# Performance work log

Measured on AMD Instinct MI355X. Metric: run time of the kernel, lower is better.

The kernel has to match this reference:

```python
import jax, jax.numpy as jnp
import numpy as np

N = 100000
E = 1600000
F_NODE = 6
F_EDGE = 2
H = 64


def _glorot(key, shape):
    lim = float(np.sqrt(6.0 / (shape[0] + shape[1])))
    return jax.random.uniform(key, shape, jnp.float32, -lim, lim)


def setup_inputs() -> dict:
    key = jax.random.key(0)
    ks = jax.random.split(key, 16)
    inp = {
        "x": jax.random.normal(ks[0], (N, F_NODE), jnp.float32),
        "edge_index": jax.random.randint(ks[1], (2, E), 0, N, jnp.int64),
        "edge_attr": jax.random.normal(ks[2], (E, F_EDGE), jnp.float32),
        # GCN layers (PyG GCNConv: linear no-bias, then aggregate, then +bias)
        "W1": _glorot(ks[3], (F_NODE, H)), "b1": jnp.zeros((H,), jnp.float32),
        "W2": _glorot(ks[4], (H, H)), "b2": jnp.zeros((H,), jnp.float32),
        "W3": _glorot(ks[5], (H, H)), "b3": jnp.zeros((H,), jnp.float32),
        # edge_mlp
        "We1": _glorot(ks[6], (F_EDGE, H)), "be1": jnp.zeros((H,), jnp.float32),
        "We2": _glorot(ks[7], (H, H)), "be2": jnp.zeros((H,), jnp.float32),
        # predictor
        "Wp1": _glorot(ks[8], (3 * H, H)), "bp1": jnp.zeros((H,), jnp.float32),
        "Wp2": _glorot(ks[9], (H, H // 2)), "bp2": jnp.zeros((H // 2,), jnp.float32),
        "Wp3": _glorot(ks[10], (H // 2, 1)), "bp3": jnp.zeros((1,), jnp.float32),
    }
    return inp


def _gcn_conv(h, W, b, src_sl, dst_sl, norm, n):
    # PyG GCNConv with self-loops and symmetric normalization
    h = h @ W                                   # [N, H_out]
    msg = h[src_sl] * norm[:, None]             # gather + scale per edge(+loop)
    out = jax.ops.segment_sum(msg, dst_sl, num_segments=n)
    return out + b


def _forward(x, edge_attr, W1, b1, W2, b2, W3, b3, We1, be1, We2, be2,
             Wp1, bp1, Wp2, bp2, Wp3, bp3, edge_index):
    n = x.shape[0]
    src, dst = edge_index[0], edge_index[1]

    # --- edge feature injection (vectorized version of per-edge loop) ---
    ef = jax.nn.relu(edge_attr @ We1 + be1) @ We2 + be2      # [E, H]
    nef = (jax.ops.segment_sum(ef, src, num_segments=n)
           + jax.ops.segment_sum(ef, dst, num_segments=n))   # [N, H]
    ones_e = jnp.ones((ef.shape[0],), x.dtype)
    deg = (jax.ops.segment_sum(ones_e, src, num_segments=n)
           + jax.ops.segment_sum(ones_e, dst, num_segments=n))
    deg = jnp.maximum(deg, 1.0)
    nef = nef / deg[:, None]
    # hidden_dim (64) >= node feature dim (6) -> truncate
    x = x + nef[:, : x.shape[1]] * 0.5

    # --- GCN normalization with self-loops (shared across layers) ---
    loop = jnp.arange(n, dtype=src.dtype)
    src_sl = jnp.concatenate([src, loop])
    dst_sl = jnp.concatenate([dst, loop])
    deg_sl = jax.ops.segment_sum(jnp.ones_like(dst_sl, dtype=x.dtype), dst_sl,
                                 num_segments=n)
    dinv = jnp.where(deg_sl > 0, deg_sl ** -0.5, 0.0)
    norm = dinv[src_sl] * dinv[dst_sl]

    h = jax.nn.relu(_gcn_conv(x, W1, b1, src_sl, dst_sl, norm, n))
    h = jax.nn.relu(_gcn_conv(h, W2, b2, src_sl, dst_sl, norm, n))
    h = _gcn_conv(h, W3, b3, src_sl, dst_sl, norm, n)

    graph_emb = h.mean(axis=0)                 # global_mean_pool, batch=None
    node_mean = h.mean(axis=0)
    node_std = jnp.std(h, axis=0, ddof=1)      # torch.std is unbiased
    combined = jnp.concatenate([graph_emb, node_mean, node_std])  # [3H]

    p = jax.nn.relu(combined @ Wp1 + bp1)      # dropout inactive in eval
    p = jax.nn.relu(p @ Wp2 + bp2)
    out = jax.nn.sigmoid(p @ Wp3 + bp3)        # (1,)
    return out


def reference(x, edge_index, edge_attr, W1, b1, W2, b2, W3, b3,
              We1, be1, We2, be2, Wp1, bp1, Wp2, bp2, Wp3, bp3):
    return _forward(x, edge_attr, W1, b1, W2, b2, W3, b3, We1, be1, We2, be2,
                    Wp1, bp1, Wp2, bp2, Wp3, bp3, edge_index)
```

## Files before the change

kernel.cpp:

```cpp
#include <hip/hip_runtime.h>
#include <hip/hip_bf16.h>
#include <stdint.h>

#define CSTRIDE 8

__device__ __forceinline__ float rdlane(float v, int l) {
    return __uint_as_float(__builtin_amdgcn_readlane(__float_as_uint(v), l));
}
__device__ __forceinline__ float bf2f(unsigned short u) {
    return __uint_as_float(((unsigned)u) << 16);
}
__device__ __forceinline__ unsigned short f2bf(float f) {
    unsigned u = __float_as_uint(f);
    u += 0x7fffu + ((u >> 16) & 1u);
    return (unsigned short)(u >> 16);
}
__device__ __forceinline__ unsigned packbf(float a, float b) {
    return (unsigned)f2bf(a) | ((unsigned)f2bf(b) << 16);
}

__global__ void k_zero(int* __restrict__ cntO, int* __restrict__ cntI,
                       double* __restrict__ sums, int n) {
    int i = blockIdx.x * blockDim.x + threadIdx.x;
    if (i < 128) sums[i] = 0.0;
    if (i < n) { cntO[(size_t)i * CSTRIDE] = 0; cntI[(size_t)i * CSTRIDE] = 0; }
}

__global__ __launch_bounds__(256) void k_front(
    const int* __restrict__ ei, const float* __restrict__ ea,
    const float* __restrict__ We1, const float* __restrict__ be1,
    const float* __restrict__ We2, const float* __restrict__ be2,
    unsigned* __restrict__ efp, int* __restrict__ cntO, int* __restrict__ cntI,
    int* __restrict__ rankS, int* __restrict__ rankD, int E) {
    __shared__ float sWe1[128], sbe1[64], sWe2[64 * 6], sbe2[6];
    int t = threadIdx.x;
    if (t < 128) sWe1[t] = We1[t];
    if (t < 64) {
        sbe1[t] = be1[t];
#pragma unroll
        for (int c = 0; c < 6; ++c) sWe2[t * 6 + c] = We2[t * 64 + c];
    }
    if (t < 6) sbe2[t] = be2[t];
    __syncthreads();

    int e = blockIdx.x * blockDim.x + t;
    if (e >= E) return;

    int s = ei[e], d = ei[E + e];
    int rs = atomicAdd(&cntO[(size_t)s * CSTRIDE], 1);
    int rd = atomicAdd(&cntI[(size_t)d * CSTRIDE], 1);

    float2 aa = ((const float2*)ea)[e];
    float a0 = aa.x, a1 = aa.y;
    float acc[6];
#pragma unroll
    for (int c = 0; c < 6; ++c) acc[c] = sbe2[c];
#pragma unroll
    for (int j = 0; j < 64; ++j) {
        float h = fmaf(a0, sWe1[j], fmaf(a1, sWe1[64 + j], sbe1[j]));
        h = fmaxf(h, 0.f);
#pragma unroll
        for (int c = 0; c < 6; ++c) acc[c] = fmaf(h, sWe2[j * 6 + c], acc[c]);
    }
    unsigned* q = efp + (size_t)e * 3;
    q[0] = packbf(acc[0], acc[1]);
    q[1] = packbf(acc[2], acc[3]);
    q[2] = packbf(acc[4], acc[5]);
    rankS[e] = rs;
    rankD[e] = rd;
}

__global__ __launch_bounds__(256) void k_scan1(const int* __restrict__ cntO,
                                               const int* __restrict__ cntI,
                                               int2* __restrict__ bsum, int n) {
    __shared__ int2 l[256];
    int i = blockIdx.x * 256 + threadIdx.x;
    l[threadIdx.x] = (i < n) ? make_int2(cntO[(size_t)i * CSTRIDE],
                                         cntI[(size_t)i * CSTRIDE])
                             : make_int2(0, 0);
    __syncthreads();
    for (int s = 128; s > 0; s >>= 1) {
        if (threadIdx.x < s) {
            l[threadIdx.x].x += l[threadIdx.x + s].x;
            l[threadIdx.x].y += l[threadIdx.x + s].y;
        }
        __syncthreads();
    }
    if (threadIdx.x == 0) bsum[blockIdx.x] = l[0];
}

__global__ __launch_bounds__(512) void k_scan2(int2* __restrict__ bsum, int nb,
                                               int* __restrict__ offON,
                                               int* __restrict__ offIN) {
    __shared__ int2 l[512];
    int t = threadIdx.x;
    int2 v = (t < nb) ? bsum[t] : make_int2(0, 0);
    l[t] = v;
    __syncthreads();
    for (int s = 1; s < 512; s <<= 1) {
        int2 tmp = (t >= s) ? l[t - s] : make_int2(0, 0);
        __syncthreads();
        l[t].x += tmp.x; l[t].y += tmp.y;
        __syncthreads();
    }
    if (t < nb) bsum[t] = make_int2(l[t].x - v.x, l[t].y - v.y);
    if (t == 511) { *offON = l[511].x; *offIN = l[511].y; }
}

__global__ __launch_bounds__(256) void k_scan3off(const int* __restrict__ cntO,
                                                  const int* __restrict__ cntI,
                                                  const int2* __restrict__ bsum,
                                                  int* __restrict__ offO,
                                                  int* __restrict__ offI, int n) {
    __shared__ int2 l[256];
    int i = blockIdx.x * 256 + threadIdx.x;
    int2 v = (i < n) ? make_int2(cntO[(size_t)i * CSTRIDE],
                                 cntI[(size_t)i * CSTRIDE])
                     : make_int2(0, 0);
    l[threadIdx.x] = v;
    __syncthreads();
    for (int s = 1; s < 256; s <<= 1) {
        int2 tmp = (threadIdx.x >= (unsigned)s) ? l[threadIdx.x - s] : make_int2(0, 0);
        __syncthreads();
        l[threadIdx.x].x += tmp.x; l[threadIdx.x].y += tmp.y;
        __syncthreads();
    }
    if (i < n) {
        int2 bs = bsum[blockIdx.x];
        offO[i] = l[threadIdx.x].x - v.x + bs.x;
        offI[i] = l[threadIdx.x].y - v.y + bs.y;
    }
}

__global__ __launch_bounds__(256) void k_place(const int* __restrict__ ei,
                                               const int* __restrict__ rankS,
                                               const int* __restrict__ rankD,
                                               const int* __restrict__ offO,
                                               const int* __restrict__ offI,
                                               unsigned* __restrict__ out_eid,
                                               uint2* __restrict__ in_pk, int E) {
    int e = blockIdx.x * blockDim.x + threadIdx.x;
    if (e >= E) return;
    int s = ei[e], d = ei[E + e];
    out_eid[offO[s] + rankS[e]] = (unsigned)e;
    in_pk[offI[d] + rankD[e]] = make_uint2((unsigned)s, (unsigned)e);
}

__global__ __launch_bounds__(256) void k_nef_x(
    const int* __restrict__ offO, const unsigned* __restrict__ out_eid,
    const int* __restrict__ offI, const uint2* __restrict__ in_pk,
    const unsigned* __restrict__ efp, const float* __restrict__ x,
    float* __restrict__ xp, float* __restrict__ dinv, int n) {
    int i = blockIdx.x * blockDim.x + threadIdx.x;
    if (i >= n) return;
    int bo = offO[i], eo = offO[i + 1];
    int bi = offI[i], eiN = offI[i + 1];
    float a0 = 0.f, a1 = 0.f, a2 = 0.f, a3 = 0.f, a4 = 0.f, a5 = 0.f;
    for (int j = bo; j < eo; ++j) {
        const unsigned* q = efp + (size_t)out_eid[j] * 3;
        unsigned u0 = q[0], u1 = q[1], u2 = q[2];
        a0 += bf2f((unsigned short)u0); a1 += bf2f((unsigned short)(u0 >> 16));
        a2 += bf2f((unsigned short)u1); a3 += bf2f((unsigned short)(u1 >> 16));
        a4 += bf2f((unsigned short)u2); a5 += bf2f((unsigned short)(u2 >> 16));
    }
    for (int j = bi; j < eiN; ++j) {
        const unsigned* q = efp + (size_t)in_pk[j].y * 3;
        unsigned u0 = q[0], u1 = q[1], u2 = q[2];
        a0 += bf2f((unsigned short)u0); a1 += bf2f((unsigned short)(u0 >> 16));
        a2 += bf2f((unsigned short)u1); a3 += bf2f((unsigned short)(u1 >> 16));
        a4 += bf2f((unsigned short)u2); a5 += bf2f((unsigned short)(u2 >> 16));
    }
    int indeg = eiN - bi;
    float degf = (float)((eo - bo) + indeg);
    float inv = 0.5f / fmaxf(degf, 1.f);
    xp[(size_t)i * 6 + 0] = x[(size_t)i * 6 + 0] + a0 * inv;
    xp[(size_t)i * 6 + 1] = x[(size_t)i * 6 + 1] + a1 * inv;
    xp[(size_t)i * 6 + 2] = x[(size_t)i * 6 + 2] + a2 * inv;
    xp[(size_t)i * 6 + 3] = x[(size_t)i * 6 + 3] + a3 * inv;
    xp[(size_t)i * 6 + 4] = x[(size_t)i * 6 + 4] + a4 * inv;
    xp[(size_t)i * 6 + 5] = x[(size_t)i * 6 + 5] + a5 * inv;
    dinv[i] = 1.f / sqrtf(1.f + (float)indeg);
}

__global__ __launch_bounds__(256) void k_mm1(const float* __restrict__ xp,
                                             const float* __restrict__ W1,
                                             const float* __restrict__ dinv,
                                             unsigned short* __restrict__ sOut, int n) {
    int lane = threadIdx.x & 63;
    int wid = (blockIdx.x * blockDim.x + threadIdx.x) >> 6;
    int nw = (gridDim.x * blockDim.x) >> 6;
    float w[6];
#pragma unroll
    for (int c = 0; c < 6; ++c) w[c] = W1[c * 64 + lane];
    for (int i = wid; i < n; i += nw) {
        float xv = (lane < 6) ? xp[(size_t)i * 6 + lane] : 0.f;
        float acc = 0.f;
#pragma unroll
        for (int c = 0; c < 6; ++c) acc = fmaf(rdlane(xv, c), w[c], acc);
        sOut[(size_t)i * 64 + lane] = f2bf(acc * dinv[i]);
    }
}

__global__ __launch_bounds__(256) void k_gathermm(
    const int* __restrict__ offI, const uint2* __restrict__ in_pk,
    const float* __restrict__ dinv, const unsigned short* __restrict__ sIn,
    const float* __restrict__ bias, const float* __restrict__ W,
    unsigned short* __restrict__ sOut, int n) {
    int lane = threadIdx.x & 63;
    int sub = lane & 15, grp = lane >> 4;
    int wid = (blockIdx.x * blockDim.x + threadIdx.x) >> 6;
    int nw = (gridDim.x * blockDim.x) >> 6;
    float w[64];
#pragma unroll
    for (int c = 0; c < 64; ++c) w[c] = W[c * 64 + lane];
    float4 bb = ((const float4*)bias)[sub];

    for (int i = wid; i < n; i += nw) {
        ushort4 sv = *(const ushort4*)(sIn + (size_t)i * 64 + sub * 4);
        float a0, a1, a2, a3;
        if (grp == 0) { a0 = bf2f(sv.x); a1 = bf2f(sv.y); a2 = bf2f(sv.z); a3 = bf2f(sv.w); }
        else { a0 = a1 = a2 = a3 = 0.f; }
        int b0 = offI[i], e0 = offI[i + 1];
#pragma unroll 4
        for (int j = b0 + grp; j < e0; j += 4) {
            unsigned src = in_pk[j].x;
            ushort4 v = *(const ushort4*)(sIn + (size_t)src * 64 + sub * 4);
            a0 += bf2f(v.x); a1 += bf2f(v.y); a2 += bf2f(v.z); a3 += bf2f(v.w);
        }
        a0 += __shfl_xor(a0, 16); a1 += __shfl_xor(a1, 16);
        a2 += __shfl_xor(a2, 16); a3 += __shfl_xor(a3, 16);
        a0 += __shfl_xor(a0, 32); a1 += __shfl_xor(a1, 32);
        a2 += __shfl_xor(a2, 32); a3 += __shfl_xor(a3, 32);

        float dv = dinv[i];
        float h0 = fmaxf(fmaf(a0, dv, bb.x), 0.f);
        float h1 = fmaxf(fmaf(a1, dv, bb.y), 0.f);
        float h2 = fmaxf(fmaf(a2, dv, bb.z), 0.f);
        float h3 = fmaxf(fmaf(a3, dv, bb.w), 0.f);
        float o = 0.f;
#pragma unroll
        for (int g = 0; g < 16; ++g) {
            o = fmaf(rdlane(h0, g), w[g * 4 + 0], o);
            o = fmaf(rdlane(h1, g), w[g * 4 + 1], o);
            o = fmaf(rdlane(h2, g), w[g * 4 + 2], o);
            o = fmaf(rdlane(h3, g), w[g * 4 + 3], o);
        }
        sOut[(size_t)i * 64 + lane] = f2bf(o * dv);
    }
}

__global__ __launch_bounds__(256) void k_gatherreduce(
    const int* __restrict__ offI, const uint2* __restrict__ in_pk,
    const float* __restrict__ dinv, const unsigned short* __restrict__ sIn,
    const float* __restrict__ b3, double* __restrict__ sums, int n) {
    int lane = threadIdx.x & 63;
    int sub = lane & 15, grp = lane >> 4;
    int wv = threadIdx.x >> 6;
    int wid = (blockIdx.x * blockDim.x + threadIdx.x) >> 6;
    int nw = (gridDim.x * blockDim.x) >> 6;
    float4 bb = ((const float4*)b3)[sub];
    double s0 = 0.0, s1 = 0.0, s2_ = 0.0, s3 = 0.0;
    double q0 = 0.0, q1 = 0.0, q2 = 0.0, q3 = 0.0;

    for (int i = wid; i < n; i += nw) {
        ushort4 sv = *(const ushort4*)(sIn + (size_t)i * 64 + sub * 4);
        float a0, a1, a2, a3;
        if (grp == 0) { a0 = bf2f(sv.x); a1 = bf2f(sv.y); a2 = bf2f(sv.z); a3 = bf2f(sv.w); }
        else { a0 = a1 = a2 = a3 = 0.f; }
        int b0 = offI[i], e0 = offI[i + 1];
#pragma unroll 4
        for (int j = b0 + grp; j < e0; j += 4) {
            unsigned src = in_pk[j].x;
            ushort4 v = *(const ushort4*)(sIn + (size_t)src * 64 + sub * 4);
            a0 += bf2f(v.x); a1 += bf2f(v.y); a2 += bf2f(v.z); a3 += bf2f(v.w);
        }
        a0 += __shfl_xor(a0, 16); a1 += __shfl_xor(a1, 16);
        a2 += __shfl_xor(a2, 16); a3 += __shfl_xor(a3, 16);
        a0 += __shfl_xor(a0, 32); a1 += __shfl_xor(a1, 32);
        a2 += __shfl_xor(a2, 32); a3 += __shfl_xor(a3, 32);

        float dv = dinv[i];
        float v0 = fmaf(a0, dv, bb.x);
        float v1 = fmaf(a1, dv, bb.y);
        float v2 = fmaf(a2, dv, bb.z);
        float v3 = fmaf(a3, dv, bb.w);
        s0 += v0; s1 += v1; s2_ += v2; s3 += v3;
        q0 += (double)v0 * v0; q1 += (double)v1 * v1;
        q2 += (double)v2 * v2; q3 += (double)v3 * v3;
    }
    __shared__ double shS[4 * 64], shQ[4 * 64];
    if (grp == 0) {
#pragma unroll
        for (int k = 0; k < 4; ++k) {
            double sk = (k == 0) ? s0 : (k == 1) ? s1 : (k == 2) ? s2_ : s3;
            double qk = (k == 0) ? q0 : (k == 1) ? q1 : (k == 2) ? q2 : q3;
            shS[wv * 64 + sub * 4 + k] = sk;
            shQ[wv * 64 + sub * 4 + k] = qk;
        }
    }
    __syncthreads();
    if (wv == 0) {
        double a = shS[lane] + shS[64 + lane] + shS[128 + lane] + shS[192 + lane];
        double c = shQ[lane] + shQ[64 + lane] + shQ[128 + lane] + shQ[192 + lane];
        unsafeAtomicAdd(&sums[lane], a);
        unsafeAtomicAdd(&sums[64 + lane], c);
    }
}

__global__ void k_head(const double* __restrict__ sums,
                       const float* __restrict__ Wp1, const float* __restrict__ bp1,
                       const float* __restrict__ Wp2, const float* __restrict__ bp2,
                       const float* __restrict__ Wp3, const float* __restrict__ bp3,
                       float* __restrict__ out, int n) {
    __shared__ float comb[192], p1[64], p2[32];
    int t = threadIdx.x;
    if (t < 64) {
        double s = sums[t], s2 = sums[64 + t];
        double m = s / n;
        double var = (s2 - s * s / n) / (double)(n - 1);
        float mf = (float)m;
        float sd = (float)sqrt(var > 0.0 ? var : 0.0);
        comb[t] = mf;
        comb[64 + t] = mf;
        comb[128 + t] = sd;
    }
    __syncthreads();
    if (t < 64) {
        float acc = bp1[t];
        for (int k = 0; k < 192; ++k) acc = fmaf(comb[k], Wp1[k * 64 + t], acc);
        p1[t] = fmaxf(acc, 0.f);
    }
    __syncthreads();
    if (t < 32) {
        float acc = bp2[t];
        for (int k = 0; k < 64; ++k) acc = fmaf(p1[k], Wp2[k * 32 + t], acc);
        p2[t] = fmaxf(acc, 0.f);
    }
    __syncthreads();
    if (t == 0) {
        float acc = bp3[0];
        for (int k = 0; k < 32; ++k) acc = fmaf(p2[k], Wp3[k], acc);
        out[0] = 1.f / (1.f + expf(-acc));
    }
}

static inline char* align16(char* p) {
    return (char*)(((uintptr_t)p + 15) & ~(uintptr_t)15);
}

extern "C" void kernel_launch(void* const* d_in, const int* in_sizes, int n_in,
                              void* d_out, int out_size, void* d_ws, size_t ws_size,
                              hipStream_t stream) {
    const float* x   = (const float*)d_in[0];
    const int*   ei  = (const int*)d_in[1];
    const float* ea  = (const float*)d_in[2];
    const float* W1  = (const float*)d_in[3];
    const float* b1  = (const float*)d_in[4];
    const float* W2  = (const float*)d_in[5];
    const float* b2  = (const float*)d_in[6];
    const float* W3  = (const float*)d_in[7];
    const float* b3  = (const float*)d_in[8];
    const float* We1 = (const float*)d_in[9];
    const float* be1 = (const float*)d_in[10];
    const float* We2 = (const float*)d_in[11];
    const float* be2 = (const float*)d_in[12];
    const float* Wp1 = (const float*)d_in[13];
    const float* bp1 = (const float*)d_in[14];
    const float* Wp2 = (const float*)d_in[15];
    const float* bp2 = (const float*)d_in[16];
    const float* Wp3 = (const float*)d_in[17];
    const float* bp3 = (const float*)d_in[18];

    const int N = in_sizes[0] / 6;
    const int E = in_sizes[1] / 2;
    const int nbN = (N + 255) / 256;
    const int nbE = (E + 255) / 256;
    const size_t SB = (size_t)N * 64 * 2;

    char* p = (char*)d_ws;
    double* sums = (double*)p;          p = align16(p + 128 * sizeof(double));
    int* cntO = (int*)p;                p = align16(p + (size_t)N * CSTRIDE * 4);
    int* cntI = (int*)p;                p = align16(p + (size_t)N * CSTRIDE * 4);
    int* offO = (int*)p;                p = align16(p + ((size_t)N + 1) * 4);
    int* offI = (int*)p;                p = align16(p + ((size_t)N + 1) * 4);
    int2* bsum = (int2*)p;              p = align16(p + 512 * 8);
    float* xp = (float*)p;              p = align16(p + (size_t)N * 6 * 4);
    float* dinv = (float*)p;            p = align16(p + (size_t)N * 4);
    uint2* in_pk = (uint2*)p;           p = align16(p + (size_t)E * 8);
    char* u1 = p;                       p = align16(p + 2 * SB);
    int* rankS = (int*)u1;
    int* rankD = (int*)(u1 + SB);
    unsigned short* sbufA = (unsigned short*)u1;
    unsigned short* sbufB = (unsigned short*)(u1 + SB);
    char* u2 = p;
    unsigned* efp = (unsigned*)u2;
    unsigned* out_eid = (unsigned*)(u2 + (size_t)E * 12);

    const int TB = 256;
    dim3 blk(TB);

    k_zero<<<dim3(nbN), blk, 0, stream>>>(cntO, cntI, sums, N);
    k_front<<<dim3(nbE), blk, 0, stream>>>(ei, ea, We1, be1, We2, be2,
                                           efp, cntO, cntI, rankS, rankD, E);
    k_scan1<<<dim3(nbN), blk, 0, stream>>>(cntO, cntI, bsum, N);
    k_scan2<<<dim3(1), dim3(512), 0, stream>>>(bsum, nbN, offO + N, offI + N);
    k_scan3off<<<dim3(nbN), blk, 0, stream>>>(cntO, cntI, bsum, offO, offI, N);
    k_place<<<dim3(nbE), blk, 0, stream>>>(ei, rankS, rankD, offO, offI, out_eid, in_pk, E);
    k_nef_x<<<dim3(nbN), blk, 0, stream>>>(offO, out_eid, offI, in_pk, efp, x, xp, dinv, N);

    k_mm1<<<dim3(1024), blk, 0, stream>>>(xp, W1, dinv, sbufA, N);
    k_gathermm<<<dim3(2048), blk, 0, stream>>>(offI, in_pk, dinv, sbufA, b1, W2, sbufB, N);
    k_gathermm<<<dim3(2048), blk, 0, stream>>>(offI, in_pk, dinv, sbufB, b2, W3, sbufA, N);
    k_gatherreduce<<<dim3(2048), blk, 0, stream>>>(offI, in_pk, dinv, sbufA, b3, sums, N);
    k_head<<<dim3(1), dim3(64), 0, stream>>>(sums, Wp1, bp1, Wp2, bp2, Wp3, bp3,
                                             (float*)d_out, N);
}
```

Measured before the change: 593.9 us.

## Store GCN node features in fp8, inline edge features into CSR records

Node feature buffers for the GCN gathers switch from bf16 to packed fp8 (4 values per 32-bit word) to halve gather traffic per edge. The placement kernel now copies each edge's packed features into the out- and in-sorted records so the nef pass reads sequentially instead of doing an indirect lookup. The per-node counter padding (stride 8) is removed, so the count arrays become dense. This trades accuracy (fp8 activations) and larger in-records (16 bytes) for less random memory traffic, and dense counters may bring more atomic contention within a cache line.

```diff
diff --git a/kernel.cpp b/kernel.cpp
--- a/kernel.cpp
+++ b/kernel.cpp
@@ -2,7 +2,7 @@
 #include <hip/hip_bf16.h>
 #include <stdint.h>
 
-#define CSTRIDE 8
+typedef float floatx2 __attribute__((ext_vector_type(2)));
 
 __device__ __forceinline__ float rdlane(float v, int l) {
     return __uint_as_float(__builtin_amdgcn_readlane(__float_as_uint(v), l));
@@ -18,12 +18,17 @@
 __device__ __forceinline__ unsigned packbf(float a, float b) {
     return (unsigned)f2bf(a) | ((unsigned)f2bf(b) << 16);
 }
+__device__ __forceinline__ unsigned pk_fp8x4(float a, float b, float c, float d) {
+    int u = __builtin_amdgcn_cvt_pk_fp8_f32(a, b, 0, false);
+    u = __builtin_amdgcn_cvt_pk_fp8_f32(c, d, u, true);
+    return (unsigned)u;
+}
 
 __global__ void k_zero(int* __restrict__ cntO, int* __restrict__ cntI,
                        double* __restrict__ sums, int n) {
     int i = blockIdx.x * blockDim.x + threadIdx.x;
     if (i < 128) sums[i] = 0.0;
-    if (i < n) { cntO[(size_t)i * CSTRIDE] = 0; cntI[(size_t)i * CSTRIDE] = 0; }
+    if (i < n) { cntO[i] = 0; cntI[i] = 0; }
 }
 
 __global__ __launch_bounds__(256) void k_front(
@@ -47,8 +52,8 @@
     if (e >= E) return;
 
     int s = ei[e], d = ei[E + e];
-    int rs = atomicAdd(&cntO[(size_t)s * CSTRIDE], 1);
-    int rd = atomicAdd(&cntI[(size_t)d * CSTRIDE], 1);
+    int rs = atomicAdd(&cntO[s], 1);
+    int rd = atomicAdd(&cntI[d], 1);
 
     float2 aa = ((const float2*)ea)[e];
     float a0 = aa.x, a1 = aa.y;
@@ -75,9 +80,7 @@
                                                int2* __restrict__ bsum, int n) {
     __shared__ int2 l[256];
     int i = blockIdx.x * 256 + threadIdx.x;
-    l[threadIdx.x] = (i < n) ? make_int2(cntO[(size_t)i * CSTRIDE],
-                                         cntI[(size_t)i * CSTRIDE])
-                             : make_int2(0, 0);
+    l[threadIdx.x] = (i < n) ? make_int2(cntO[i], cntI[i]) : make_int2(0, 0);
     __syncthreads();
     for (int s = 128; s > 0; s >>= 1) {
         if (threadIdx.x < s) {
@@ -114,9 +117,7 @@
                                                   int* __restrict__ offI, int n) {
     __shared__ int2 l[256];
     int i = blockIdx.x * 256 + threadIdx.x;
-    int2 v = (i < n) ? make_int2(cntO[(size_t)i * CSTRIDE],
-                                 cntI[(size_t)i * CSTRIDE])
-                     : make_int2(0, 0);
+    int2 v = (i < n) ? make_int2(cntO[i], cntI[i]) : make_int2(0, 0);
     l[threadIdx.x] = v;
     __syncthreads();
     for (int s = 1; s < 256; s <<= 1) {
@@ -137,19 +138,23 @@
                                                const int* __restrict__ rankD,
                                                const int* __restrict__ offO,
                                                const int* __restrict__ offI,
-                                               unsigned* __restrict__ out_eid,
-                                               uint2* __restrict__ in_pk, int E) {
+                                               const unsigned* __restrict__ efp,
+                                               unsigned* __restrict__ out_rec,
+                                               uint4* __restrict__ in_rec, int E) {
     int e = blockIdx.x * blockDim.x + threadIdx.x;
     if (e >= E) return;
     int s = ei[e], d = ei[E + e];
-    out_eid[offO[s] + rankS[e]] = (unsigned)e;
-    in_pk[offI[d] + rankD[e]] = make_uint2((unsigned)s, (unsigned)e);
+    const unsigned* q = efp + (size_t)e * 3;
+    unsigned u0 = q[0], u1 = q[1], u2 = q[2];
+    size_t so = (size_t)(offO[s] + rankS[e]) * 3;
+    out_rec[so] = u0; out_rec[so + 1] = u1; out_rec[so + 2] = u2;
+    in_rec[offI[d] + rankD[e]] = make_uint4((unsigned)s, u0, u1, u2);
 }
 
 __global__ __launch_bounds__(256) void k_nef_x(
-    const int* __restrict__ offO, const unsigned* __restrict__ out_eid,
-    const int* __restrict__ offI, const uint2* __restrict__ in_pk,
-    const unsigned* __restrict__ efp, const float* __restrict__ x,
+    const int* __restrict__ offO, const unsigned* __restrict__ out_rec,
+    const int* __restrict__ offI, const uint4* __restrict__ in_rec,
+    const float* __restrict__ x,
     float* __restrict__ xp, float* __restrict__ dinv, int n) {
     int i = blockIdx.x * blockDim.x + threadIdx.x;
     if (i >= n) return;
@@ -157,18 +162,17 @@
     int bi = offI[i], eiN = offI[i + 1];
     float a0 = 0.f, a1 = 0.f, a2 = 0.f, a3 = 0.f, a4 = 0.f, a5 = 0.f;
     for (int j = bo; j < eo; ++j) {
-        const unsigned* q = efp + (size_t)out_eid[j] * 3;
+        const unsigned* q = out_rec + (size_t)j * 3;
         unsigned u0 = q[0], u1 = q[1], u2 = q[2];
         a0 += bf2f((unsigned short)u0); a1 += bf2f((unsigned short)(u0 >> 16));
         a2 += bf2f((unsigned short)u1); a3 += bf2f((unsigned short)(u1 >> 16));
         a4 += bf2f((unsigned short)u2); a5 += bf2f((unsigned short)(u2 >> 16));
     }
     for (int j = bi; j < eiN; ++j) {
-        const unsigned* q = efp + (size_t)in_pk[j].y * 3;
-        unsigned u0 = q[0], u1 = q[1], u2 = q[2];
-        a0 += bf2f((unsigned short)u0); a1 += bf2f((unsigned short)(u0 >> 16));
-        a2 += bf2f((unsigned short)u1); a3 += bf2f((unsigned short)(u1 >> 16));
-        a4 += bf2f((unsigned short)u2); a5 += bf2f((unsigned short)(u2 >> 16));
+        uint4 r = in_rec[j];
+        a0 += bf2f((unsigned short)r.y); a1 += bf2f((unsigned short)(r.y >> 16));
+        a2 += bf2f((unsigned short)r.z); a3 += bf2f((unsigned short)(r.z >> 16));
+        a4 += bf2f((unsigned short)r.w); a5 += bf2f((unsigned short)(r.w >> 16));
     }
     int indeg = eiN - bi;
     float degf = (float)((eo - bo) + indeg);
@@ -185,8 +189,9 @@
 __global__ __launch_bounds__(256) void k_mm1(const float* __restrict__ xp,
                                              const float* __restrict__ W1,
                                              const float* __restrict__ dinv,
-                                             unsigned short* __restrict__ sOut, int n) {
+                                             unsigned* __restrict__ sOut, int n) {
     int lane = threadIdx.x & 63;
+    int sub = lane & 15;
     int wid = (blockIdx.x * blockDim.x + threadIdx.x) >> 6;
     int nw = (gridDim.x * blockDim.x) >> 6;
     float w[6];
@@ -197,15 +202,20 @@
         float acc = 0.f;
 #pragma unroll
         for (int c = 0; c < 6; ++c) acc = fmaf(rdlane(xv, c), w[c], acc);
-        sOut[(size_t)i * 64 + lane] = f2bf(acc * dinv[i]);
+        float o = acc * dinv[i];
+        float o0 = __shfl(o, sub * 4 + 0);
+        float o1 = __shfl(o, sub * 4 + 1);
+        float o2 = __shfl(o, sub * 4 + 2);
+        float o3 = __shfl(o, sub * 4 + 3);
+        if (lane < 16) sOut[(size_t)i * 16 + lane] = pk_fp8x4(o0, o1, o2, o3);
     }
 }
 
 __global__ __launch_bounds__(256) void k_gathermm(
-    const int* __restrict__ offI, const uint2* __restrict__ in_pk,
-    const float* __restrict__ dinv, const unsigned short* __restrict__ sIn,
+    const int* __restrict__ offI, const uint4* __restrict__ in_rec,
+    const float* __restrict__ dinv, const unsigned* __restrict__ sIn,
     const float* __restrict__ bias, const float* __restrict__ W,
-    unsigned short* __restrict__ sOut, int n) {
+    unsigned* __restrict__ sOut, int n) {
     int lane = threadIdx.x & 63;
     int sub = lane & 15, grp = lane >> 4;
     int wid = (blockIdx.x * blockDim.x + threadIdx.x) >> 6;
@@ -216,16 +226,21 @@
     float4 bb = ((const float4*)bias)[sub];
 
     for (int i = wid; i < n; i += nw) {
-        ushort4 sv = *(const ushort4*)(sIn + (size_t)i * 64 + sub * 4);
+        unsigned su = sIn[(size_t)i * 16 + sub];
         float a0, a1, a2, a3;
-        if (grp == 0) { a0 = bf2f(sv.x); a1 = bf2f(sv.y); a2 = bf2f(sv.z); a3 = bf2f(sv.w); }
-        else { a0 = a1 = a2 = a3 = 0.f; }
+        if (grp == 0) {
+            floatx2 lo = __builtin_amdgcn_cvt_pk_f32_fp8(su, false);
+            floatx2 hi = __builtin_amdgcn_cvt_pk_f32_fp8(su, true);
+            a0 = lo.x; a1 = lo.y; a2 = hi.x; a3 = hi.y;
+        } else { a0 = a1 = a2 = a3 = 0.f; }
         int b0 = offI[i], e0 = offI[i + 1];
 #pragma unroll 4
         for (int j = b0 + grp; j < e0; j += 4) {
-            unsigned src = in_pk[j].x;
-            ushort4 v = *(const ushort4*)(sIn + (size_t)src * 64 + sub * 4);
-            a0 += bf2f(v.x); a1 += bf2f(v.y); a2 += bf2f(v.z); a3 += bf2f(v.w);
+            unsigned src = in_rec[j].x;
+            unsigned u = sIn[(size_t)src * 16 + sub];
+            floatx2 lo = __builtin_amdgcn_cvt_pk_f32_fp8(u, false);
+            floatx2 hi = __builtin_amdgcn_cvt_pk_f32_fp8(u, true);
+            a0 += lo.x; a1 += lo.y; a2 += hi.x; a3 += hi.y;
         }
         a0 += __shfl_xor(a0, 16); a1 += __shfl_xor(a1, 16);
         a2 += __shfl_xor(a2, 16); a3 += __shfl_xor(a3, 16);
@@ -245,13 +260,18 @@
             o = fmaf(rdlane(h2, g), w[g * 4 + 2], o);
             o = fmaf(rdlane(h3, g), w[g * 4 + 3], o);
         }
-        sOut[(size_t)i * 64 + lane] = f2bf(o * dv);
+        o *= dv;
+        float o0 = __shfl(o, sub * 4 + 0);
+        float o1 = __shfl(o, sub * 4 + 1);
+        float o2 = __shfl(o, sub * 4 + 2);
+        float o3 = __shfl(o, sub * 4 + 3);
+        if (lane < 16) sOut[(size_t)i * 16 + lane] = pk_fp8x4(o0, o1, o2, o3);
     }
 }
 
 __global__ __launch_bounds__(256) void k_gatherreduce(
-    const int* __restrict__ offI, const uint2* __restrict__ in_pk,
-    const float* __restrict__ dinv, const unsigned short* __restrict__ sIn,
+    const int* __restrict__ offI, const uint4* __restrict__ in_rec,
+    const float* __restrict__ dinv, const unsigned* __restrict__ sIn,
     const float* __restrict__ b3, double* __restrict__ sums, int n) {
     int lane = threadIdx.x & 63;
     int sub = lane & 15, grp = lane >> 4;
@@ -263,16 +283,21 @@
     double q0 = 0.0, q1 = 0.0, q2 = 0.0, q3 = 0.0;
 
     for (int i = wid; i < n; i += nw) {
-        ushort4 sv = *(const ushort4*)(sIn + (size_t)i * 64 + sub * 4);
+        unsigned su = sIn[(size_t)i * 16 + sub];
         float a0, a1, a2, a3;
-        if (grp == 0) { a0 = bf2f(sv.x); a1 = bf2f(sv.y); a2 = bf2f(sv.z); a3 = bf2f(sv.w); }
-        else { a0 = a1 = a2 = a3 = 0.f; }
+        if (grp == 0) {
+            floatx2 lo = __builtin_amdgcn_cvt_pk_f32_fp8(su, false);
+            floatx2 hi = __builtin_amdgcn_cvt_pk_f32_fp8(su, true);
+            a0 = lo.x; a1 = lo.y; a2 = hi.x; a3 = hi.y;
+        } else { a0 = a1 = a2 = a3 = 0.f; }
         int b0 = offI[i], e0 = offI[i + 1];
 #pragma unroll 4
         for (int j = b0 + grp; j < e0; j += 4) {
-            unsigned src = in_pk[j].x;
-            ushort4 v = *(const ushort4*)(sIn + (size_t)src * 64 + sub * 4);
-            a0 += bf2f(v.x); a1 += bf2f(v.y); a2 += bf2f(v.z); a3 += bf2f(v.w);
+            unsigned src = in_rec[j].x;
+            unsigned u = sIn[(size_t)src * 16 + sub];
+            floatx2 lo = __builtin_amdgcn_cvt_pk_f32_fp8(u, false);
+            floatx2 hi = __builtin_amdgcn_cvt_pk_f32_fp8(u, true);
+            a0 += lo.x; a1 += lo.y; a2 += hi.x; a3 += hi.y;
         }
         a0 += __shfl_xor(a0, 16); a1 += __shfl_xor(a1, 16);
         a2 += __shfl_xor(a2, 16); a3 += __shfl_xor(a3, 16);
@@ -375,26 +400,26 @@
     const int E = in_sizes[1] / 2;
     const int nbN = (N + 255) / 256;
     const int nbE = (E + 255) / 256;
-    const size_t SB = (size_t)N * 64 * 2;
+    const size_t SB = (size_t)N * 64;
 
     char* p = (char*)d_ws;
     double* sums = (double*)p;          p = align16(p + 128 * sizeof(double));
-    int* cntO = (int*)p;                p = align16(p + (size_t)N * CSTRIDE * 4);
-    int* cntI = (int*)p;                p = align16(p + (size_t)N * CSTRIDE * 4);
+    int* cntO = (int*)p;                p = align16(p + (size_t)N * 4);
+    int* cntI = (int*)p;                p = align16(p + (size_t)N * 4);
     int* offO = (int*)p;                p = align16(p + ((size_t)N + 1) * 4);
     int* offI = (int*)p;                p = align16(p + ((size_t)N + 1) * 4);
     int2* bsum = (int2*)p;              p = align16(p + 512 * 8);
     float* xp = (float*)p;              p = align16(p + (size_t)N * 6 * 4);
     float* dinv = (float*)p;            p = align16(p + (size_t)N * 4);
-    uint2* in_pk = (uint2*)p;           p = align16(p + (size_t)E * 8);
-    char* u1 = p;                       p = align16(p + 2 * SB);
+    uint4* in_rec = (uint4*)p;          p = align16(p + (size_t)E * 16);
+    char* u1 = p;                       p = align16(p + 2 * ((SB + 15) & ~(size_t)15));
     int* rankS = (int*)u1;
-    int* rankD = (int*)(u1 + SB);
-    unsigned short* sbufA = (unsigned short*)u1;
-    unsigned short* sbufB = (unsigned short*)(u1 + SB);
+    int* rankD = (int*)(u1 + ((SB + 15) & ~(size_t)15));
+    unsigned* sbufA = (unsigned*)rankS;
+    unsigned* sbufB = (unsigned*)rankD;
     char* u2 = p;
     unsigned* efp = (unsigned*)u2;
-    unsigned* out_eid = (unsigned*)(u2 + (size_t)E * 12);
+    unsigned* out_rec = (unsigned*)(u2 + (size_t)E * 12);
 
     const int TB = 256;
     dim3 blk(TB);
@@ -405,13 +430,14 @@
     k_scan1<<<dim3(nbN), blk, 0, stream>>>(cntO, cntI, bsum, N);
     k_scan2<<<dim3(1), dim3(512), 0, stream>>>(bsum, nbN, offO + N, offI + N);
     k_scan3off<<<dim3(nbN), blk, 0, stream>>>(cntO, cntI, bsum, offO, offI, N);
-    k_place<<<dim3(nbE), blk, 0, stream>>>(ei, rankS, rankD, offO, offI, out_eid, in_pk, E);
-    k_nef_x<<<dim3(nbN), blk, 0, stream>>>(offO, out_eid, offI, in_pk, efp, x, xp, dinv, N);
+    k_place<<<dim3(nbE), blk, 0, stream>>>(ei, rankS, rankD, offO, offI, efp,
+                                           out_rec, in_rec, E);
+    k_nef_x<<<dim3(nbN), blk, 0, stream>>>(offO, out_rec, offI, in_rec, x, xp, dinv, N);
 
     k_mm1<<<dim3(1024), blk, 0, stream>>>(xp, W1, dinv, sbufA, N);
-    k_gathermm<<<dim3(2048), blk, 0, stream>>>(offI, in_pk, dinv, sbufA, b1, W2, sbufB, N);
-    k_gathermm<<<dim3(2048), blk, 0, stream>>>(offI, in_pk, dinv, sbufB, b2, W3, sbufA, N);
-    k_gatherreduce<<<dim3(2048), blk, 0, stream>>>(offI, in_pk, dinv, sbufA, b3, sums, N);
+    k_gathermm<<<dim3(2048), blk, 0, stream>>>(offI, in_rec, dinv, sbufA, b1, W2, sbufB, N);
+    k_gathermm<<<dim3(2048), blk, 0, stream>>>(offI, in_rec, dinv, sbufB, b2, W3, sbufA, N);
+    k_gatherreduce<<<dim3(2048), blk, 0, stream>>>(offI, in_rec, dinv, sbufA, b3, sums, N);
     k_head<<<dim3(1), dim3(64), 0, stream>>>(sums, Wp1, bp1, Wp2, bp2, Wp3, bp3,
                                              (float*)d_out, N);
 }
```

After: 543.8 us. 1.09x faster.
